# Optimization experiments

Hardware: AMD Instinct MI355X
Metric: run time of the kernel (lower is better)

## Reference

```python
import jax, jax.numpy as jnp
import numpy as np

USER_NUM, ITEM_NUM = 50000, 25000
N_U, N_I = 4096, 4096
N_E, N_PRED = 262144, 65536
D, K, N_LAYERS = 64, 1000, 3
SSL_TEMP, SSL_REG, ALPHA, PROTO_REG = 0.1, 1e-6, 1.0, 8e-8


def setup_inputs() -> dict:
    key = jax.random.key(0)
    ks = jax.random.split(key, 16)
    return {
        "emb_user": jax.random.normal(ks[0], (USER_NUM, D), jnp.float32),
        "emb_item": jax.random.normal(ks[1], (ITEM_NUM, D), jnp.float32),
        "user_centroids": jax.random.normal(ks[2], (K, D), jnp.float32),
        "item_centroids": jax.random.normal(ks[3], (K, D), jnp.float32),
        "edge_u": jax.random.randint(ks[4], (N_E,), 0, N_U, jnp.int32),
        "edge_v": jax.random.randint(ks[5], (N_E,), 0, N_I, jnp.int32),
        "pos_u": jax.random.randint(ks[6], (N_PRED,), 0, N_U, jnp.int32),
        "pos_v": jax.random.randint(ks[7], (N_PRED,), 0, N_I, jnp.int32),
        "neg_u": jax.random.randint(ks[8], (N_PRED,), 0, N_U, jnp.int32),
        "neg_v": jax.random.randint(ks[9], (N_PRED,), 0, N_I, jnp.int32),
        "idx_user": jax.random.randint(ks[10], (N_U,), 0, USER_NUM, jnp.int32),
        "idx_item": jax.random.randint(ks[11], (N_I,), 0, ITEM_NUM, jnp.int32),
        "user2cluster": jax.random.randint(ks[12], (USER_NUM,), 0, K, jnp.int32),
        "item2cluster": jax.random.randint(ks[13], (ITEM_NUM,), 0, K, jnp.int32),
    }


def _l2norm(x, eps=1e-12):  # F.normalize(p=2, dim=1)
    return x / jnp.maximum(jnp.linalg.norm(x, axis=1, keepdims=True), eps)


def _ssl_loss(cur, prev, prev_total):
    nc, npv, nt = _l2norm(cur), _l2norm(prev), _l2norm(prev_total)
    pos = jnp.exp(jnp.sum(nc * npv, axis=1) / SSL_TEMP)            # [B]
    tot = jnp.exp(nc @ nt.T / SSL_TEMP).sum(axis=1)                 # [B]
    return -jnp.log(pos / tot).sum()


def _proto_loss(emb, idx, node2cluster, centroids):
    ne = _l2norm(emb)
    cents = _l2norm(centroids)                                      # run_kmeans normalizes centroids
    my_cent = cents[node2cluster[idx]]                              # [B, D]
    pos = jnp.exp(jnp.sum(ne * my_cent, axis=1) / SSL_TEMP)
    tot = jnp.exp(ne @ cents.T / SSL_TEMP).sum(axis=1)
    return -jnp.log(pos / tot).sum()


def reference(emb_user, emb_item, user_centroids, item_centroids,
              edge_u, edge_v, pos_u, pos_v, neg_u, neg_v,
              idx_user, idx_item, user2cluster, item2cluster):
    # --- symmetric-normalized bipartite GraphConv (norm='both', no weight/bias) ---
    ones_e = jnp.ones((N_E,), jnp.float32)
    deg_u = jax.ops.segment_sum(ones_e, edge_u, num_segments=N_U)
    deg_i = jax.ops.segment_sum(ones_e, edge_v, num_segments=N_I)
    inv_u = (1.0 / jnp.sqrt(jnp.maximum(deg_u, 1.0)))[:, None]      # [N_U,1]
    inv_i = (1.0 / jnp.sqrt(jnp.maximum(deg_i, 1.0)))[:, None]      # [N_I,1]

    e_u = emb_user[idx_user]                                        # initial subgraph embeddings
    e_i = emb_item[idx_item]
    res_u, res_i = e_u, e_i
    h_u, h_i = e_u, e_i
    for _ in range(N_LAYERS):
        m_u = (h_u * inv_u)[edge_u]                                 # messages along rate edges
        m_i = (h_i * inv_i)[edge_v]                                 # messages along rated-by edges
        new_i = jax.ops.segment_sum(m_u, edge_v, num_segments=N_I) * inv_i
        new_u = jax.ops.segment_sum(m_i, edge_u, num_segments=N_U) * inv_u
        h_u, h_i = new_u, new_i
        res_u = res_u + h_u
        res_i = res_i + h_i

    # --- structural-neighbour SSL loss (last layer output vs layer-0 embeddings) ---
    ssl_u = _ssl_loss(h_u, e_u, emb_user)
    ssl_i = _ssl_loss(h_i, e_i, emb_item)
    ssl_loss = SSL_REG * (ssl_u + ALPHA * ssl_i)

    # --- protoNCE loss (raw embedding-table rows vs kmeans centroids) ---
    proto_loss = PROTO_REG * (
        _proto_loss(emb_user[idx_user], idx_user, user2cluster, user_centroids)
        + _proto_loss(emb_item[idx_item], idx_item, item2cluster, item_centroids)
    )

    res_u = res_u / (N_LAYERS + 1)
    res_i = res_i / (N_LAYERS + 1)

    # --- HeteroDotProductPredictor: u_dot_v on 'rate' edges -> [E,1] ---
    pos_score = jnp.sum(res_u[pos_u] * res_i[pos_v], axis=1, keepdims=True)
    neg_score = jnp.sum(res_u[neg_u] * res_i[neg_v], axis=1, keepdims=True)
    return pos_score, neg_score, ssl_loss, proto_loss
```

## Files before the change

### kernel.cpp

```cpp
#include <hip/hip_runtime.h>
#include <hip/hip_bf16.h>

#define NU 4096
#define NI 4096
#define NE 262144
#define NPRED 65536
#define DD 64
#define KCL 1000
#define UNUM 50000
#define INUM 25000
#define NUPAD 50016
#define NIPAD 25024
#define NKPAD 1024

typedef short sh8 __attribute__((ext_vector_type(8)));
typedef float f4 __attribute__((ext_vector_type(4)));

__device__ __forceinline__ float wred64(float x){
#pragma unroll
  for(int m=1;m<64;m<<=1) x += __shfl_xor(x,m);
  return x;
}

__device__ __forceinline__ float fast_exp2(float x){
  return __builtin_amdgcn_exp2f(x);
}

__global__ void k_hist(const int* __restrict__ eu, const int* __restrict__ ev,
                       int* cu, int* ci){
  int t = blockIdx.x*256 + threadIdx.x;
  if(t < NE){ atomicAdd(&cu[eu[t]],1); atomicAdd(&ci[ev[t]],1); }
}

__global__ void k_scan(const int* cnt_u, int* rp_u, int* cur_u, float* inv_u,
                       const int* cnt_i, int* rp_i, int* cur_i, float* inv_i,
                       float* tot4){
  {
    int base = blockIdx.x*8192 + threadIdx.x*8;
#pragma unroll
    for(int k=0;k<8;k++) tot4[base+k] = 0.f;
  }
  const int* cnt = blockIdx.x ? cnt_i : cnt_u;
  int* rp  = blockIdx.x ? rp_i  : rp_u;
  int* cur = blockIdx.x ? cur_i : cur_u;
  float* inv = blockIdx.x ? inv_i : inv_u;
  __shared__ int sdata[1024];
  int tid = threadIdx.x;
  int v[4]; int s = 0;
#pragma unroll
  for(int k=0;k<4;k++){ v[k]=cnt[tid*4+k]; s+=v[k]; }
  sdata[tid]=s; __syncthreads();
  for(int off=1; off<1024; off<<=1){
    int add = (tid>=off)? sdata[tid-off] : 0;
    __syncthreads();
    if(tid>=off) sdata[tid] += add;
    __syncthreads();
  }
  int run = sdata[tid]-s;
#pragma unroll
  for(int k=0;k<4;k++){
    int idx = tid*4+k;
    rp[idx]=run; cur[idx]=run;
    inv[idx] = 1.0f/sqrtf(fmaxf((float)v[k],1.0f));
    run += v[k];
  }
  if(tid==1023) rp[4096]=run;
}

__global__ void k_fillgather(const int* __restrict__ eu, const int* __restrict__ ev,
                             int* cur_u, int* cur_i, int* adj_u, int* adj_i,
                             const float* __restrict__ emb_u, const float* __restrict__ emb_i,
                             const int* __restrict__ idx_u, const int* __restrict__ idx_i,
                             const float* __restrict__ inv_u, const float* __restrict__ inv_i,
                             float* e_u, float* e_i, float* res_u, float* res_i,
                             float* hs_u, float* hs_i){
  int b = blockIdx.x;
  if(b < 1024){
    int t = b*256 + threadIdx.x;
    int u=eu[t], v=ev[t];
    adj_u[atomicAdd(&cur_u[u],1)] = v;
    adj_i[atomicAdd(&cur_i[v],1)] = u;
  } else {
    int t = (b-1024)*256 + threadIdx.x;
    const int half = NU*DD;
    if(t < half){
      int r=t>>6;
      float v = emb_u[idx_u[r]*DD + (t&63)];
      e_u[t]=v; res_u[t]=v; hs_u[t]=v*inv_u[r];
    } else {
      int s=t-half; int r=s>>6;
      float v = emb_i[idx_i[r]*DD + (s&63)];
      e_i[s]=v; res_i[s]=v; hs_i[s]=v*inv_i[r];
    }
  }
}

__global__ void k_conv(const int* __restrict__ rp_i, const int* __restrict__ adj_i,
                       const float* __restrict__ hsu_in, const float* __restrict__ inv_i,
                       float* h_i, float* res_i, float* hsi_out,
                       const int* __restrict__ rp_u, const int* __restrict__ adj_u,
                       const float* __restrict__ hsi_in, const float* __restrict__ inv_u,
                       float* h_u, float* res_u, float* hsu_out){
  int b = blockIdx.x*4 + (threadIdx.x>>6);
  int lane = threadIdx.x & 63;
  const int* rp; const int* adj; const float* srcv; const float* inv;
  float *h, *res, *hso; int node;
  if(b < NI){ rp=rp_i; adj=adj_i; srcv=hsu_in; inv=inv_i; h=h_i; res=res_i; hso=hsi_out; node=b; }
  else      { node=b-NI; rp=rp_u; adj=adj_u; srcv=hsi_in; inv=inv_u; h=h_u; res=res_u; hso=hsu_out; }
  int s=rp[node], e=rp[node+1];
  float acc=0.f;
  for(int base=s; base<e; base+=64){
    int m = e-base;
    int myidx = adj[base + min(lane, m-1)];
    int kk = min(64, m);
    int k=0;
    for(; k+8<=kk; k+=8){
      int i0=__shfl(myidx,k  ), i1=__shfl(myidx,k+1),
          i2=__shfl(myidx,k+2), i3=__shfl(myidx,k+3),
          i4=__shfl(myidx,k+4), i5=__shfl(myidx,k+5),
          i6=__shfl(myidx,k+6), i7=__shfl(myidx,k+7);
      float v0=srcv[i0*DD+lane], v1=srcv[i1*DD+lane],
            v2=srcv[i2*DD+lane], v3=srcv[i3*DD+lane],
            v4=srcv[i4*DD+lane], v5=srcv[i5*DD+lane],
            v6=srcv[i6*DD+lane], v7=srcv[i7*DD+lane];
      acc += ((v0+v1)+(v2+v3)) + ((v4+v5)+(v6+v7));
    }
    for(; k<kk; k++) acc += srcv[__shfl(myidx,k)*DD+lane];
  }
  float iv = inv[node];
  float outv = acc*iv;
  h[node*DD+lane] = outv;
  res[node*DD+lane] += outv;
  hso[node*DD+lane] = outv*iv;
}

#define SB0 12504
#define SB1 (SB0+6256)
#define SB2 (SB1+256)
#define SB3 (SB2+256)
#define SB4 (SB3+1024)
#define SB5 (SB4+1024)
#define SB6 (SB5+1024)
#define SB7 (SB6+1024)

__global__ void k_normpos(const float* __restrict__ emb_u, const float* __restrict__ emb_i,
                          const float* __restrict__ ucent, const float* __restrict__ icent,
                          const float* __restrict__ h_u, const float* __restrict__ h_i,
                          const float* __restrict__ e_u, const float* __restrict__ e_i,
                          __hip_bfloat16* ntb_u, __hip_bfloat16* ntb_i,
                          __hip_bfloat16* ncb_u, __hip_bfloat16* ncb_i,
                          __hip_bfloat16* nc_u, __hip_bfloat16* nc_i,
                          __hip_bfloat16* npv_u, __hip_bfloat16* npv_i,
                          const int* __restrict__ idx_u, const int* __restrict__ idx_i,
                          const int* __restrict__ u2c, const int* __restrict__ i2c,
                          float* pos4){
  const float SC = 14.426950408889634f;
  int b = blockIdx.x;
  int lane = threadIdx.x & 63;
  if(b >= SB7){
    int w = (b-SB7)*4 + (threadIdx.x>>6);
    float hu=h_u[w*DD+lane], eu=e_u[w*DD+lane];
    float hi=h_i[w*DD+lane], ei=e_i[w*DD+lane];
    int cu = u2c[idx_u[w]], ci = i2c[idx_i[w]];
    float cuv = ucent[cu*DD+lane], civ = icent[ci*DD+lane];
    float hh = wred64(hu*hu), ee = wred64(eu*eu), he = wred64(hu*eu);
    float h2 = wred64(hi*hi), e2 = wred64(ei*ei), hei= wred64(hi*ei);
    float ccu= wred64(cuv*cuv), ecu = wred64(eu*cuv);
    float cci= wred64(civ*civ), eci = wred64(ei*civ);
    if(lane==0){
      const float eps=1e-12f;
      pos4[0*NU+w] = he  / (fmaxf(sqrtf(hh),eps)*fmaxf(sqrtf(ee),eps));
      pos4[1*NU+w] = hei / (fmaxf(sqrtf(h2),eps)*fmaxf(sqrtf(e2),eps));
      pos4[2*NU+w] = ecu / (fmaxf(sqrtf(ee),eps)*fmaxf(sqrtf(ccu),eps));
      pos4[3*NU+w] = eci / (fmaxf(sqrtf(e2),eps)*fmaxf(sqrtf(cci),eps));
    }
    return;
  }
  const float* in; __hip_bfloat16* outp; int rows; float scale; int base;
  if(b < SB0)      { in=emb_u; outp=ntb_u; rows=UNUM; scale=1.f;  base=0; }
  else if(b < SB1) { in=emb_i; outp=ntb_i; rows=INUM; scale=1.f;  base=SB0; }
  else if(b < SB2) { in=ucent; outp=ncb_u; rows=KCL;  scale=1.f;  base=SB1; }
  else if(b < SB3) { in=icent; outp=ncb_i; rows=KCL;  scale=1.f;  base=SB2; }
  else if(b < SB4) { in=h_u;   outp=nc_u;  rows=NU;   scale=SC;   base=SB3; }
  else if(b < SB5) { in=h_i;   outp=nc_i;  rows=NI;   scale=SC;   base=SB4; }
  else if(b < SB6) { in=e_u;   outp=npv_u; rows=NU;   scale=SC;   base=SB5; }
  else             { in=e_i;   outp=npv_i; rows=NI;   scale=SC;   base=SB6; }
  int row = (b-base)*4 + (threadIdx.x>>6);
  if(row >= rows){
    outp[row*DD + lane] = __float2bfloat16(0.f);
    return;
  }
  float v = in[row*DD + lane];
  float s = wred64(v*v);
  float sc = scale / fmaxf(sqrtf(s), 1e-12f);
  outp[row*DD + lane] = __float2bfloat16(v*sc);
}

#define ECH 256
#define EUU 1568
#define EUI (EUU+784)
#define EUP0 (EUI+32)
#define EUP1 (EUP0+32)
#define NSU 8192
#define UTOT (EUP1+NSU)

struct ESeg { const __hip_bfloat16* A; const __hip_bfloat16* B; float* tot; int nB; };
struct SArg { const float* res_u; const float* res_i;
              const int* pu; const int* pv; const int* nu; const int* nv; float* out; };

__global__ __launch_bounds__(256,3)
void k_expscore(ESeg s0, ESeg s1, ESeg s2, ESeg s3, SArg sc){
  int tid = threadIdx.x;
  int wave = tid >> 6;
  int lane = tid & 63;
  int r = lane & 15, kq = (lane>>4)*8;

  for(int u = blockIdx.x; u < UTOT; u += 1024){
    if(u < EUP1){
      ESeg s; int rem;
      if(u < EUU)       { s = s0; rem = u; }
      else if(u < EUI)  { s = s1; rem = u-EUU; }
      else if(u < EUP0) { s = s2; rem = u-EUI; }
      else              { s = s3; rem = u-EUP0; }
      int yc = rem >> 3, x = rem & 7;
      int row0 = (x*4 + wave)*128;
      int j_begin = yc*ECH;
      int j_end = min(j_begin + ECH, s.nB);

      sh8 a0[8], a1[8];
#pragma unroll
      for(int t=0;t<8;t++){
        const short* ap = (const short*)(s.A + (row0 + t*16 + r)*DD);
        a0[t] = *(const sh8*)(ap + kq);
        a1[t] = *(const sh8*)(ap + kq + 32);
      }
      float acc[8][4];
#pragma unroll
      for(int t=0;t<8;t++)
#pragma unroll
        for(int q=0;q<4;q++) acc[t][q]=0.f;

      const short* bbase = (const short*)s.B;
      const short* bp = bbase + (j_begin + r)*DD + kq;
      sh8 b0 = *(const sh8*)(bp);
      sh8 b1 = *(const sh8*)(bp + 32);
      sh8 b2 = *(const sh8*)(bp + 16*DD);
      sh8 b3 = *(const sh8*)(bp + 16*DD + 32);

#pragma unroll 1
      for(int j0=j_begin; j0<j_end; j0+=32){
        const short* np = bbase + (j0 + 32 + r)*DD + kq;
        sh8 n0 = *(const sh8*)(np);
        sh8 n1 = *(const sh8*)(np + 32);
        sh8 n2 = *(const sh8*)(np + 16*DD);
        sh8 n3 = *(const sh8*)(np + 16*DD + 32);
#pragma unroll
        for(int t=0;t<8;t++){
          f4 c0 = {0.f,0.f,0.f,0.f};
          f4 c1 = {0.f,0.f,0.f,0.f};
          c0 = __builtin_amdgcn_mfma_f32_16x16x32_bf16(a0[t], b0, c0, 0,0,0);
          c1 = __builtin_amdgcn_mfma_f32_16x16x32_bf16(a0[t], b2, c1, 0,0,0);
          c0 = __builtin_amdgcn_mfma_f32_16x16x32_bf16(a1[t], b1, c0, 0,0,0);
          c1 = __builtin_amdgcn_mfma_f32_16x16x32_bf16(a1[t], b3, c1, 0,0,0);
#pragma unroll
          for(int q=0;q<4;q++)
            acc[t][q] += fast_exp2(c0[q]) + fast_exp2(c1[q]);
        }
        b0 = n0; b1 = n1; b2 = n2; b3 = n3;
      }
#pragma unroll
      for(int t=0;t<8;t++){
#pragma unroll
        for(int q=0;q<4;q++){
          float v = acc[t][q];
          v += __shfl_xor(v,1); v += __shfl_xor(v,2);
          v += __shfl_xor(v,4); v += __shfl_xor(v,8);
          if(r==0) atomicAdd(&s.tot[row0 + t*16 + (lane>>4)*4 + q], v);
        }
      }
    } else {
      int u2 = u - EUP1;
      int pair = u2*16 + (tid>>4);
      int sl = tid & 15;
      int a,b;
      if(pair < NPRED){ a=sc.pu[pair]; b=sc.pv[pair]; }
      else { a=sc.nu[pair-NPRED]; b=sc.nv[pair-NPRED]; }
      f4 xu = *(const f4*)(sc.res_u + a*DD + sl*4);
      f4 xv = *(const f4*)(sc.res_i + b*DD + sl*4);
      float x = xu[0]*xv[0] + xu[1]*xv[1] + xu[2]*xv[2] + xu[3]*xv[3];
      x += __shfl_xor(x,1); x += __shfl_xor(x,2);
      x += __shfl_xor(x,4); x += __shfl_xor(x,8);
      if(sl==0) sc.out[pair] = x*(1.0f/16.0f);
    }
  }
}

__global__ void k_loss(const float* __restrict__ tot4, const float* __restrict__ pos4,
                       float* out){
  const float PU_ = (float)(NUPAD-UNUM);
  const float PI_ = (float)(NIPAD-INUM);
  const float PK_ = (float)(NKPAD-KCL);
  float s0=0,s1=0,s2=0,s3=0;
  for(int b=threadIdx.x; b<NU; b+=256){
    s0 += logf(tot4[0*NU+b] - PU_) - 10.f*pos4[0*NU+b];
    s1 += logf(tot4[1*NU+b] - PI_) - 10.f*pos4[1*NU+b];
    s2 += logf(tot4[2*NU+b] - PK_) - 10.f*pos4[2*NU+b];
    s3 += logf(tot4[3*NU+b] - PK_) - 10.f*pos4[3*NU+b];
  }
  s0=wred64(s0); s1=wred64(s1); s2=wred64(s2); s3=wred64(s3);
  __shared__ float ls[4][4];
  int lane=threadIdx.x&63, w=threadIdx.x>>6;
  if(lane==0){ ls[w][0]=s0; ls[w][1]=s1; ls[w][2]=s2; ls[w][3]=s3; }
  __syncthreads();
  if(threadIdx.x==0){
    float a=0,b2=0,c=0,d=0;
#pragma unroll
    for(int k=0;k<4;k++){ a+=ls[k][0]; b2+=ls[k][1]; c+=ls[k][2]; d+=ls[k][3]; }
    out[2*NPRED]   = 1e-6f*(a+b2);
    out[2*NPRED+1] = 8e-8f*(c+d);
  }
}

extern "C" void kernel_launch(void* const* d_in, const int* in_sizes, int n_in,
                              void* d_out, int out_size, void* d_ws, size_t ws_size,
                              hipStream_t stream) {
  const float* emb_user = (const float*)d_in[0];
  const float* emb_item = (const float*)d_in[1];
  const float* ucent    = (const float*)d_in[2];
  const float* icent    = (const float*)d_in[3];
  const int* edge_u = (const int*)d_in[4];
  const int* edge_v = (const int*)d_in[5];
  const int* pos_u  = (const int*)d_in[6];
  const int* pos_v  = (const int*)d_in[7];
  const int* neg_u  = (const int*)d_in[8];
  const int* neg_v  = (const int*)d_in[9];
  const int* idx_u  = (const int*)d_in[10];
  const int* idx_i  = (const int*)d_in[11];
  const int* u2c    = (const int*)d_in[12];
  const int* i2c    = (const int*)d_in[13];
  float* out = (float*)d_out;

  char* w = (char*)d_ws;
  auto alloc = [&](size_t bytes)->void*{
    void* p = (void*)w;
    w += (bytes + 255) & ~(size_t)255;
    return p;
  };
  int* cnt_u = (int*)alloc(NU*4);
  int* cnt_i = (int*)alloc(NI*4);
  int* rp_u  = (int*)alloc((NU+1)*4);
  int* rp_i  = (int*)alloc((NI+1)*4);
  int* cur_u = (int*)alloc(NU*4);
  int* cur_i = (int*)alloc(NI*4);
  int* adj_u = (int*)alloc((size_t)NE*4);
  int* adj_i = (int*)alloc((size_t)NE*4);
  float* inv_u = (float*)alloc(NU*4);
  float* inv_i = (float*)alloc(NI*4);
  float* e_u  = (float*)alloc((size_t)NU*DD*4);
  float* e_i  = (float*)alloc((size_t)NI*DD*4);
  float* h_u  = (float*)alloc((size_t)NU*DD*4);
  float* h_i  = (float*)alloc((size_t)NI*DD*4);
  float* hsA_u = (float*)alloc((size_t)NU*DD*4);
  float* hsA_i = (float*)alloc((size_t)NI*DD*4);
  float* hsB_u = (float*)alloc((size_t)NU*DD*4);
  float* hsB_i = (float*)alloc((size_t)NI*DD*4);
  float* res_u= (float*)alloc((size_t)NU*DD*4);
  float* res_i= (float*)alloc((size_t)NI*DD*4);
  __hip_bfloat16* ntb_user = (__hip_bfloat16*)alloc((size_t)(NUPAD+64)*DD*2);
  __hip_bfloat16* ntb_item = (__hip_bfloat16*)alloc((size_t)(NIPAD+64)*DD*2);
  __hip_bfloat16* ncb_u = (__hip_bfloat16*)alloc((size_t)(NKPAD+64)*DD*2);
  __hip_bfloat16* ncb_i = (__hip_bfloat16*)alloc((size_t)(NKPAD+64)*DD*2);
  __hip_bfloat16* nc_u  = (__hip_bfloat16*)alloc((size_t)NU*DD*2);
  __hip_bfloat16* nc_i  = (__hip_bfloat16*)alloc((size_t)NI*DD*2);
  __hip_bfloat16* npv_u = (__hip_bfloat16*)alloc((size_t)NU*DD*2);
  __hip_bfloat16* npv_i = (__hip_bfloat16*)alloc((size_t)NI*DD*2);
  float* tot4 = (float*)alloc(4*NU*4);
  float* pos4 = (float*)alloc(4*NU*4);

  hipMemsetAsync(cnt_u, 0, 2*NU*4, stream);

  k_hist<<<NE/256, 256, 0, stream>>>(edge_u, edge_v, cnt_u, cnt_i);
  k_scan<<<2, 1024, 0, stream>>>(cnt_u, rp_u, cur_u, inv_u,
                                 cnt_i, rp_i, cur_i, inv_i, tot4);
  k_fillgather<<<3072, 256, 0, stream>>>(edge_u, edge_v, cur_u, cur_i, adj_u, adj_i,
                                         emb_user, emb_item, idx_u, idx_i,
                                         inv_u, inv_i,
                                         e_u, e_i, res_u, res_i, hsA_u, hsA_i);
  k_conv<<<(NU+NI)/4, 256, 0, stream>>>(rp_i, adj_i, hsA_u, inv_i, h_i, res_i, hsB_i,
                                        rp_u, adj_u, hsA_i, inv_u, h_u, res_u, hsB_u);
  k_conv<<<(NU+NI)/4, 256, 0, stream>>>(rp_i, adj_i, hsB_u, inv_i, h_i, res_i, hsA_i,
                                        rp_u, adj_u, hsB_i, inv_u, h_u, res_u, hsA_u);
  k_conv<<<(NU+NI)/4, 256, 0, stream>>>(rp_i, adj_i, hsA_u, inv_i, h_i, res_i, hsB_i,
                                        rp_u, adj_u, hsA_i, inv_u, h_u, res_u, hsB_u);

  k_normpos<<<SB7+NU/4, 256, 0, stream>>>(emb_user, emb_item, ucent, icent,
                                          h_u, h_i, e_u, e_i,
                                          ntb_user, ntb_item, ncb_u, ncb_i,
                                          nc_u, nc_i, npv_u, npv_i,
                                          idx_u, idx_i, u2c, i2c, pos4);

  ESeg su = { nc_u,  ntb_user, tot4 + 0*NU, NUPAD };
  ESeg si = { nc_i,  ntb_item, tot4 + 1*NU, NIPAD };
  ESeg sp0= { npv_u, ncb_u,    tot4 + 2*NU, NKPAD };
  ESeg sp1= { npv_i, ncb_i,    tot4 + 3*NU, NKPAD };
  SArg sc = { res_u, res_i, pos_u, pos_v, neg_u, neg_v, out };
  k_expscore<<<1024, 256, 0, stream>>>(su, si, sp0, sp1, sc);

  k_loss<<<1, 256, 0, stream>>>(tot4, pos4, out);
}
```

Measured before the change: 257.5 us.

## Stage B tiles into LDS via async global_load_lds double buffering; split score kernel

```diff
diff --git a/kernel.cpp b/kernel.cpp
--- a/kernel.cpp
+++ b/kernel.cpp
@@ -9,8 +9,8 @@
 #define KCL 1000
 #define UNUM 50000
 #define INUM 25000
-#define NUPAD 50016
-#define NIPAD 25024
+#define NUPAD 50048
+#define NIPAD 25088
 #define NKPAD 1024
 
 typedef short sh8 __attribute__((ext_vector_type(8)));
@@ -24,6 +24,11 @@
 
 __device__ __forceinline__ float fast_exp2(float x){
   return __builtin_amdgcn_exp2f(x);
+}
+
+__device__ __forceinline__ void gload_lds16(const void* g, void* l){
+  __builtin_amdgcn_global_load_lds((const __attribute__((address_space(1))) void*)g,
+                                   (__attribute__((address_space(3))) void*)l, 16, 0, 0);
 }
 
 __global__ void k_hist(const int* __restrict__ eu, const int* __restrict__ ev,
@@ -134,8 +139,8 @@
   hso[node*DD+lane] = outv*iv;
 }
 
-#define SB0 12504
-#define SB1 (SB0+6256)
+#define SB0 12512
+#define SB1 (SB0+6272)
 #define SB2 (SB1+256)
 #define SB3 (SB2+256)
 #define SB4 (SB3+1024)
@@ -196,103 +201,109 @@
   outp[row*DD + lane] = __float2bfloat16(v*sc);
 }
 
-#define ECH 256
-#define EUU 1568
-#define EUI (EUU+784)
-#define EUP0 (EUI+32)
-#define EUP1 (EUP0+32)
-#define NSU 8192
-#define UTOT (EUP1+NSU)
-
-struct ESeg { const __hip_bfloat16* A; const __hip_bfloat16* B; float* tot; int nB; };
-struct SArg { const float* res_u; const float* res_i;
-              const int* pu; const int* pv; const int* nu; const int* nv; float* out; };
+#define ECH 128
+#define EUU 3128
+#define EUI (EUU+1568)
+#define EUP0 (EUI+64)
+#define EUP1 (EUP0+64)
+#define EGRID 768
+
+struct ESeg { const __hip_bfloat16* A; const __hip_bfloat16* B; float* tot; int pad; };
 
 __global__ __launch_bounds__(256,3)
-void k_expscore(ESeg s0, ESeg s1, ESeg s2, ESeg s3, SArg sc){
+void k_expsum(ESeg s0, ESeg s1, ESeg s2, ESeg s3){
+  __shared__ __hip_bfloat16 sB[2][ECH*DD];
   int tid = threadIdx.x;
   int wave = tid >> 6;
   int lane = tid & 63;
   int r = lane & 15, kq = (lane>>4)*8;
 
-  for(int u = blockIdx.x; u < UTOT; u += 1024){
-    if(u < EUP1){
-      ESeg s; int rem;
-      if(u < EUU)       { s = s0; rem = u; }
-      else if(u < EUI)  { s = s1; rem = u-EUU; }
-      else if(u < EUP0) { s = s2; rem = u-EUI; }
-      else              { s = s3; rem = u-EUP0; }
-      int yc = rem >> 3, x = rem & 7;
-      int row0 = (x*4 + wave)*128;
-      int j_begin = yc*ECH;
-      int j_end = min(j_begin + ECH, s.nB);
-
-      sh8 a0[8], a1[8];
-#pragma unroll
-      for(int t=0;t<8;t++){
-        const short* ap = (const short*)(s.A + (row0 + t*16 + r)*DD);
-        a0[t] = *(const sh8*)(ap + kq);
-        a1[t] = *(const sh8*)(ap + kq + 32);
-      }
-      float acc[8][4];
-#pragma unroll
-      for(int t=0;t<8;t++)
-#pragma unroll
-        for(int q=0;q<4;q++) acc[t][q]=0.f;
-
-      const short* bbase = (const short*)s.B;
-      const short* bp = bbase + (j_begin + r)*DD + kq;
+  auto resolve = [&](int u, ESeg& s, int& yc, int& x){
+    int rem;
+    if(u < EUU)       { s = s0; rem = u; }
+    else if(u < EUI)  { s = s1; rem = u-EUU; }
+    else if(u < EUP0) { s = s2; rem = u-EUI; }
+    else              { s = s3; rem = u-EUP0; }
+    yc = rem >> 3; x = rem & 7;
+  };
+  auto stage = [&](const __hip_bfloat16* B, int j_begin, int buf){
+    const __hip_bfloat16* src = B + (size_t)(j_begin + wave*32 + (lane>>3))*DD + (lane&7)*8;
+#pragma unroll
+    for(int i=0;i<4;i++){
+      gload_lds16((const void*)(src + i*8*DD), (void*)&sB[buf][(wave*32 + i*8)*DD]);
+    }
+  };
+
+  { ESeg s; int yc, x; resolve(blockIdx.x, s, yc, x); stage(s.B, yc*ECH, 0); }
+  int cur = 0;
+
+  for(int u = blockIdx.x; u < EUP1; u += EGRID){
+    ESeg s; int yc, x; resolve(u, s, yc, x);
+    __syncthreads();
+    if(u + EGRID < EUP1){
+      ESeg sn; int ycn, xn; resolve(u+EGRID, sn, ycn, xn);
+      stage(sn.B, ycn*ECH, cur^1);
+    }
+    int row0 = (x*4 + wave)*128;
+    sh8 a0[8], a1[8];
+#pragma unroll
+    for(int t=0;t<8;t++){
+      const short* ap = (const short*)(s.A + (row0 + t*16 + r)*DD);
+      a0[t] = *(const sh8*)(ap + kq);
+      a1[t] = *(const sh8*)(ap + kq + 32);
+    }
+    float acc[8][4];
+#pragma unroll
+    for(int t=0;t<8;t++)
+#pragma unroll
+      for(int q=0;q<4;q++) acc[t][q]=0.f;
+
+    const short* sbase = (const short*)&sB[cur][0];
+#pragma unroll 2
+    for(int j0=0; j0<ECH; j0+=16){
+      const short* bp = sbase + (j0 + r)*DD + kq;
       sh8 b0 = *(const sh8*)(bp);
       sh8 b1 = *(const sh8*)(bp + 32);
-      sh8 b2 = *(const sh8*)(bp + 16*DD);
-      sh8 b3 = *(const sh8*)(bp + 16*DD + 32);
-
-#pragma unroll 1
-      for(int j0=j_begin; j0<j_end; j0+=32){
-        const short* np = bbase + (j0 + 32 + r)*DD + kq;
-        sh8 n0 = *(const sh8*)(np);
-        sh8 n1 = *(const sh8*)(np + 32);
-        sh8 n2 = *(const sh8*)(np + 16*DD);
-        sh8 n3 = *(const sh8*)(np + 16*DD + 32);
-#pragma unroll
-        for(int t=0;t<8;t++){
-          f4 c0 = {0.f,0.f,0.f,0.f};
-          f4 c1 = {0.f,0.f,0.f,0.f};
-          c0 = __builtin_amdgcn_mfma_f32_16x16x32_bf16(a0[t], b0, c0, 0,0,0);
-          c1 = __builtin_amdgcn_mfma_f32_16x16x32_bf16(a0[t], b2, c1, 0,0,0);
-          c0 = __builtin_amdgcn_mfma_f32_16x16x32_bf16(a1[t], b1, c0, 0,0,0);
-          c1 = __builtin_amdgcn_mfma_f32_16x16x32_bf16(a1[t], b3, c1, 0,0,0);
-#pragma unroll
-          for(int q=0;q<4;q++)
-            acc[t][q] += fast_exp2(c0[q]) + fast_exp2(c1[q]);
-        }
-        b0 = n0; b1 = n1; b2 = n2; b3 = n3;
+#pragma unroll
+      for(int t=0;t<8;t++){
+        f4 c = {0.f,0.f,0.f,0.f};
+        c = __builtin_amdgcn_mfma_f32_16x16x32_bf16(a0[t], b0, c, 0,0,0);
+        c = __builtin_amdgcn_mfma_f32_16x16x32_bf16(a1[t], b1, c, 0,0,0);
+#pragma unroll
+        for(int q=0;q<4;q++) acc[t][q] += fast_exp2(c[q]);
       }
-#pragma unroll
-      for(int t=0;t<8;t++){
-#pragma unroll
-        for(int q=0;q<4;q++){
-          float v = acc[t][q];
-          v += __shfl_xor(v,1); v += __shfl_xor(v,2);
-          v += __shfl_xor(v,4); v += __shfl_xor(v,8);
-          if(r==0) atomicAdd(&s.tot[row0 + t*16 + (lane>>4)*4 + q], v);
-        }
+    }
+#pragma unroll
+    for(int t=0;t<8;t++){
+#pragma unroll
+      for(int q=0;q<4;q++){
+        float v = acc[t][q];
+        v += __shfl_xor(v,1); v += __shfl_xor(v,2);
+        v += __shfl_xor(v,4); v += __shfl_xor(v,8);
+        if(r==0) atomicAdd(&s.tot[row0 + t*16 + (lane>>4)*4 + q], v);
       }
-    } else {
-      int u2 = u - EUP1;
-      int pair = u2*16 + (tid>>4);
-      int sl = tid & 15;
-      int a,b;
-      if(pair < NPRED){ a=sc.pu[pair]; b=sc.pv[pair]; }
-      else { a=sc.nu[pair-NPRED]; b=sc.nv[pair-NPRED]; }
-      f4 xu = *(const f4*)(sc.res_u + a*DD + sl*4);
-      f4 xv = *(const f4*)(sc.res_i + b*DD + sl*4);
-      float x = xu[0]*xv[0] + xu[1]*xv[1] + xu[2]*xv[2] + xu[3]*xv[3];
-      x += __shfl_xor(x,1); x += __shfl_xor(x,2);
-      x += __shfl_xor(x,4); x += __shfl_xor(x,8);
-      if(sl==0) sc.out[pair] = x*(1.0f/16.0f);
-    }
-  }
+    }
+    cur ^= 1;
+  }
+}
+
+__global__ void k_score(const float* __restrict__ res_u, const float* __restrict__ res_i,
+                        const int* __restrict__ pu, const int* __restrict__ pv,
+                        const int* __restrict__ nu, const int* __restrict__ nv,
+                        float* out){
+  int t = blockIdx.x*256 + threadIdx.x;
+  int pair = t >> 4;
+  int sl = t & 15;
+  if(pair >= 2*NPRED) return;
+  int a,b;
+  if(pair < NPRED){ a=pu[pair]; b=pv[pair]; }
+  else { a=nu[pair-NPRED]; b=nv[pair-NPRED]; }
+  f4 xu = *(const f4*)(res_u + a*DD + sl*4);
+  f4 xv = *(const f4*)(res_i + b*DD + sl*4);
+  float x = xu[0]*xv[0] + xu[1]*xv[1] + xu[2]*xv[2] + xu[3]*xv[3];
+  x += __shfl_xor(x,1); x += __shfl_xor(x,2);
+  x += __shfl_xor(x,4); x += __shfl_xor(x,8);
+  if(sl==0) out[pair] = x*(1.0f/16.0f);
 }
 
 __global__ void k_loss(const float* __restrict__ tot4, const float* __restrict__ pos4,
@@ -366,10 +377,10 @@
   float* hsB_i = (float*)alloc((size_t)NI*DD*4);
   float* res_u= (float*)alloc((size_t)NU*DD*4);
   float* res_i= (float*)alloc((size_t)NI*DD*4);
-  __hip_bfloat16* ntb_user = (__hip_bfloat16*)alloc((size_t)(NUPAD+64)*DD*2);
-  __hip_bfloat16* ntb_item = (__hip_bfloat16*)alloc((size_t)(NIPAD+64)*DD*2);
-  __hip_bfloat16* ncb_u = (__hip_bfloat16*)alloc((size_t)(NKPAD+64)*DD*2);
-  __hip_bfloat16* ncb_i = (__hip_bfloat16*)alloc((size_t)(NKPAD+64)*DD*2);
+  __hip_bfloat16* ntb_user = (__hip_bfloat16*)alloc((size_t)NUPAD*DD*2);
+  __hip_bfloat16* ntb_item = (__hip_bfloat16*)alloc((size_t)NIPAD*DD*2);
+  __hip_bfloat16* ncb_u = (__hip_bfloat16*)alloc((size_t)NKPAD*DD*2);
+  __hip_bfloat16* ncb_i = (__hip_bfloat16*)alloc((size_t)NKPAD*DD*2);
   __hip_bfloat16* nc_u  = (__hip_bfloat16*)alloc((size_t)NU*DD*2);
   __hip_bfloat16* nc_i  = (__hip_bfloat16*)alloc((size_t)NI*DD*2);
   __hip_bfloat16* npv_u = (__hip_bfloat16*)alloc((size_t)NU*DD*2);
@@ -399,12 +410,12 @@
                                           nc_u, nc_i, npv_u, npv_i,
                                           idx_u, idx_i, u2c, i2c, pos4);
 
-  ESeg su = { nc_u,  ntb_user, tot4 + 0*NU, NUPAD };
-  ESeg si = { nc_i,  ntb_item, tot4 + 1*NU, NIPAD };
-  ESeg sp0= { npv_u, ncb_u,    tot4 + 2*NU, NKPAD };
-  ESeg sp1= { npv_i, ncb_i,    tot4 + 3*NU, NKPAD };
-  SArg sc = { res_u, res_i, pos_u, pos_v, neg_u, neg_v, out };
-  k_expscore<<<1024, 256, 0, stream>>>(su, si, sp0, sp1, sc);
-
+  ESeg su = { nc_u,  ntb_user, tot4 + 0*NU, 0 };
+  ESeg si = { nc_i,  ntb_item, tot4 + 1*NU, 0 };
+  ESeg sp0= { npv_u, ncb_u,    tot4 + 2*NU, 0 };
+  ESeg sp1= { npv_i, ncb_i,    tot4 + 3*NU, 0 };
+  k_expsum<<<EGRID, 256, 0, stream>>>(su, si, sp0, sp1);
+
+  k_score<<<(2*NPRED*16)/256, 256, 0, stream>>>(res_u, res_i, pos_u, pos_v, neg_u, neg_v, out);
   k_loss<<<1, 256, 0, stream>>>(tot4, pos4, out);
 }
```

New measurement: 256.1 us, median of 2. No clear change (-0.5%).
